# Kernel tuning notes

Hardware: AMD Instinct MI355X
Metric: run time of the kernel (lower is better)

Reference implementation:

```python
import jax, jax.numpy as jnp
import numpy as np

B, C_IN, H, W = 2, 128, 96, 320
CQ = C_IN // 4   # q/k channels = 32
D = 32           # number of disparities


def _groupnorm1(x, w, b, eps=1e-5):
    # GroupNorm with 1 group == LayerNorm over (C,H,W) per sample, per-channel affine
    mu = x.mean(axis=(1, 2, 3), keepdims=True)
    var = x.var(axis=(1, 2, 3), keepdims=True)
    return (x - mu) / jnp.sqrt(var + eps) * w[None, :, None, None] + b[None, :, None, None]


def _warp_volume(x, disp, directs):
    # Faithful to affine_grid + grid_sample(bilinear, border, align_corners=True)
    # with a pure horizontal shift: pixel offset = disp * direct * (W-1).
    Bx, C, Hx, Wx = x.shape
    d = directs.reshape(Bx, 1, 1)                       # [B,1,1]
    j = jnp.arange(Wx, dtype=x.dtype)
    pos = j[None, None, :] + disp[None, :, None] * d * (Wx - 1)   # [B,D,W]
    pos = jnp.clip(pos, 0.0, Wx - 1)                    # border padding
    x0 = jnp.clip(jnp.floor(pos).astype(jnp.int32), 0, Wx - 1)
    x1 = jnp.minimum(x0 + 1, Wx - 1)
    t = pos - x0.astype(x.dtype)                        # [B,D,W]

    def per_b(xb, i0, i1, tb):
        g0 = xb[:, :, i0]                                # [C,H,D,W]
        g1 = xb[:, :, i1]
        return g0 * (1.0 - tb) + g1 * tb

    warped = jax.vmap(per_b)(x, x0, x1, t)               # [B,C,H,D,W]
    return jnp.moveaxis(warped, 3, 4)                    # [B,C,H,W,D]


def setup_inputs() -> dict:
    key = jax.random.key(0)
    ks = jax.random.split(key, 12)
    s = lambda i, shape: jax.random.normal(ks[i], shape, jnp.float32) * 0.05
    return {
        "t_feat": jax.random.normal(ks[0], (B, C_IN, H, W), jnp.float32),
        "s_feat": jax.random.normal(ks[1], (B, C_IN, H, W), jnp.float32),
        "directs": jnp.ones((B, 1, 1, 1), jnp.float32),
        "disp": jnp.arange(D, dtype=jnp.float32) * 0.01,   # norm_disp_range
        "q_w": s(2, (CQ, C_IN)), "q_b": jnp.zeros((CQ,), jnp.float32),
        "k_w": s(3, (CQ, C_IN)), "k_b": jnp.zeros((CQ,), jnp.float32),
        "cf_w": s(4, (1, 1, 3, 3, 3)), "cf_b": jnp.zeros((1,), jnp.float32),
        "nt_w": jnp.ones((C_IN,), jnp.float32), "nt_b": jnp.zeros((C_IN,), jnp.float32),
        "nc_w": jnp.ones((D,), jnp.float32), "nc_b": jnp.zeros((D,), jnp.float32),
        "ce_w": s(5, (C_IN, D)), "ce_b": jnp.zeros((C_IN,), jnp.float32),
        "fa_w": s(6, (1, 2 * C_IN)), "fa_b": jnp.zeros((1,), jnp.float32),
        "rc_w": s(7, (C_IN, C_IN, 3, 3)), "rc_b": jnp.zeros((C_IN,), jnp.float32),
        "se_w1": s(8, (C_IN // 16, C_IN)),
        "se_w2": s(9, (C_IN, C_IN // 16)),
    }


def reference(t_feat, s_feat, directs, disp, q_w, q_b, k_w, k_b, cf_w, cf_b,
              nt_w, nt_b, nc_w, nc_b, ce_w, ce_b, fa_w, fa_b, rc_w, rc_b,
              se_w1, se_w2):
    eps = 1e-12
    # 1x1 q/k projections
    q = jnp.einsum('oc,bchw->bohw', q_w, t_feat) + q_b[None, :, None, None]
    k = jnp.einsum('oc,bchw->bohw', k_w, s_feat) + k_b[None, :, None, None]

    # per-disparity warp -> [B,Cq,H,W,D]
    warped = _warp_volume(k, disp, directs)

    # DAV with patch_size=1: per-pixel cosine similarity over channels
    qn = q / jnp.maximum(jnp.linalg.norm(q, axis=1, keepdims=True), eps)
    kn = warped / jnp.maximum(jnp.linalg.norm(warped, axis=1, keepdims=True), eps)
    sim = jnp.einsum('bchw,bchwd->bdhw', qn, kn)          # [B,D,H,W]

    # 3x3x3 cost filter (Conv3d 1->1, padding 1)
    cost = jax.lax.conv_general_dilated(
        sim[:, None], cf_w, (1, 1, 1), [(1, 1)] * 3,
        dimension_numbers=('NCDHW', 'OIDHW', 'NCDHW'))[:, 0] + cf_b[0]
    norm_cost = jax.nn.softmax(cost, axis=1)              # softmax over D

    t_n = _groupnorm1(t_feat, nt_w, nt_b)
    c_n = _groupnorm1(norm_cost, nc_w, nc_b)
    cost_feat = jnp.einsum('od,bdhw->bohw', ce_w, c_n) + ce_b[None, :, None, None]

    fusion_in = jnp.concatenate([t_n, cost_feat], axis=1)
    alpha = jax.nn.sigmoid(jnp.einsum('oc,bchw->bohw', fa_w, fusion_in)
                           + fa_b[None, :, None, None])
    fused = alpha * t_n + (1.0 - alpha) * cost_feat       # same spatial size, no interp

    # redu: reflection-pad 3x3 conv -> SE -> ELU
    xp = jnp.pad(fused, ((0, 0), (0, 0), (1, 1), (1, 1)), mode='reflect')
    x = jax.lax.conv_general_dilated(
        xp, rc_w, (1, 1), 'VALID',
        dimension_numbers=('NCHW', 'OIHW', 'NCHW')) + rc_b[None, :, None, None]
    y = x.mean(axis=(2, 3))                               # [B,C]
    y = jax.nn.relu(y @ se_w1.T)
    y = jax.nn.sigmoid(y @ se_w2.T)
    x = jax.nn.elu(x * y[:, :, None, None])
    return (x, norm_cost)
```

## Files before the change

### kernel.cpp

```cpp
#include <hip/hip_runtime.h>
#include <stdint.h>

#define CC    128
#define CQn   32
#define DD    32
#define IMG_H 96
#define IMG_W 320
#define HW    30720
#define NPIX  61440

#define OFF_Q     0
#define OFF_K     3932160
#define OFF_SIM   7864320
#define OFF_NCP   15728640
#define OFF_FUSED 0
#define OFF_WC    19660800
#define OFF_WQK   19955712
#define OFF_AP    19972096
#define OFF_MISC  19988480
#define OFF_ST    20000768

typedef _Float16 half_t;
typedef _Float16 f16x2 __attribute__((ext_vector_type(2)));
typedef _Float16 f16x8 __attribute__((ext_vector_type(8)));
typedef float    f32x4 __attribute__((ext_vector_type(4)));

__device__ __forceinline__ float fdot2f(f16x2 a, f16x2 b, float c){
#if __has_builtin(__builtin_amdgcn_fdot2)
  return __builtin_amdgcn_fdot2(a, b, c, false);
#else
  return c + (float)a.x*(float)b.x + (float)a.y*(float)b.y;
#endif
}

__global__ __launch_bounds__(256) void k0_prep(
    const float* __restrict__ rc_w, const float* __restrict__ q_w, const float* __restrict__ k_w,
    const float* __restrict__ ce_w, const float* __restrict__ ce_b,
    const float* __restrict__ fa_w, const float* __restrict__ nt_w, const float* __restrict__ nt_b,
    half_t* __restrict__ wconv, half_t* __restrict__ wqk, float* __restrict__ gbuf){
  int blk = blockIdx.x, tid = threadIdx.x;
  if (blk < 576){
    int idx = blk * 256 + tid;
    int j = idx & 7;
    int o = (idx >> 3) & 127;
    int g = idx >> 10;
    int kq = g & 3, q4 = (g >> 2) & 3, pos = g >> 4;
    int c = q4*32 + kq*8 + j;
    wconv[idx] = (half_t)rc_w[(o*128 + c)*9 + pos];
  } else if (blk < 608){
    int idx = (blk - 576) * 256 + tid;
    wqk[idx] = (half_t)(idx < 4096 ? q_w[idx] : k_w[idx - 4096]);
  } else {
    int t = tid;
    if (t < 32){
      float a = 0.f;
      for (int o = 0; o < 128; o++) a += fa_w[128 + o] * ce_w[o * 32 + t];
      gbuf[t] = a;
    } else if (t == 32){
      float a = 0.f;
      for (int o = 0; o < 128; o++) a += fa_w[128 + o] * ce_b[o];
      gbuf[32] = a;
    } else if (t == 33){
      float a = 0.f;
      for (int c = 0; c < 128; c++) a += fa_w[c] * nt_w[c];
      gbuf[33] = a;
    } else if (t == 34){
      float a = 0.f;
      for (int c = 0; c < 128; c++) a += fa_w[c] * nt_b[c];
      gbuf[34] = a;
    }
  }
}

__global__ __launch_bounds__(256) void k1_qk(
    const float* __restrict__ t_feat, const float* __restrict__ s_feat,
    const half_t* __restrict__ wqk, const float* __restrict__ q_b, const float* __restrict__ k_b,
    half_t* __restrict__ qbuf, half_t* __restrict__ kbuf,
    double* __restrict__ tsum, double* __restrict__ tsq){
  __shared__ half_t feat[128 * 136];
  __shared__ float red1[4], red2[4];
  __shared__ float qbl[32], kbl[32];
  int tid = threadIdx.x;
  int b = blockIdx.x / 240;
  int pix0 = (blockIdx.x % 240) * 128;
  int lane = tid & 63, wid = tid >> 6;
  int quad = lane >> 4, l15 = lane & 15;
  if (tid < 32){ qbl[tid] = q_b[tid]; kbl[tid] = k_b[tid]; }
  int px_s = tid & 127, hf = tid >> 7;

  for (int phase = 0; phase < 2; phase++){
    const float* src = (phase == 0 ? t_feat : s_feat) + (size_t)b * CC * HW + pix0 + px_s;
    float s1 = 0.f, s2 = 0.f;
    for (int c = hf * 64; c < hf * 64 + 64; c += 2){
      float v0 = src[c * HW], v1 = src[(c + 1) * HW];
      if (phase == 0){ s1 += v0 + v1; s2 += v0 * v0 + v1 * v1; }
      *(f16x2*)&feat[px_s * 136 + c] = f16x2{(half_t)v0, (half_t)v1};
    }
    if (phase == 0){
      #pragma unroll
      for (int off = 32; off > 0; off >>= 1){ s1 += __shfl_down(s1, off, 64); s2 += __shfl_down(s2, off, 64); }
      if (lane == 0){ red1[wid] = s1; red2[wid] = s2; }
    }
    __syncthreads();
    if (phase == 0 && tid == 0){
      atomicAdd(&tsum[b], (double)red1[0] + red1[1] + red1[2] + red1[3]);
      atomicAdd(&tsq[b],  (double)red2[0] + red2[1] + red2[2] + red2[3]);
    }
    const half_t* W = wqk + phase * 4096;
    f32x4 acc[2][2];
    #pragma unroll
    for (int m = 0; m < 2; m++){ acc[m][0] = (f32x4){0,0,0,0}; acc[m][1] = (f32x4){0,0,0,0}; }
    #pragma unroll
    for (int q4 = 0; q4 < 4; q4++){
      f16x8 a0 = *(const f16x8*)&W[(l15) * 128 + q4*32 + quad*8];
      f16x8 a1 = *(const f16x8*)&W[(16 + l15) * 128 + q4*32 + quad*8];
      #pragma unroll
      for (int nt = 0; nt < 2; nt++){
        f16x8 bf = *(const f16x8*)&feat[(wid*32 + nt*16 + l15) * 136 + q4*32 + quad*8];
        acc[0][nt] = __builtin_amdgcn_mfma_f32_16x16x32_f16(a0, bf, acc[0][nt], 0, 0, 0);
        acc[1][nt] = __builtin_amdgcn_mfma_f32_16x16x32_f16(a1, bf, acc[1][nt], 0, 0, 0);
      }
    }
    const float* bl = phase == 0 ? qbl : kbl;
    #pragma unroll
    for (int m = 0; m < 2; m++)
      #pragma unroll
      for (int nt = 0; nt < 2; nt++)
        #pragma unroll
        for (int r = 0; r < 4; r++){
          int o = m*16 + quad*4 + r;
          feat[(wid*32 + nt*16 + l15) * 136 + o] = (half_t)(acc[m][nt][r] + bl[o]);
        }
    __syncthreads();
    {
      half_t* dst = (phase == 0 ? qbuf : kbuf) + (size_t)(b * HW + pix0 + px_s) * 32;
      if (hf == 0){
        uint4* d4 = (uint4*)dst;
        const uint4* s4 = (const uint4*)&feat[px_s * 136];
        d4[0] = s4[0]; d4[1] = s4[1]; d4[2] = s4[2]; d4[3] = s4[3];
      }
    }
    __syncthreads();
  }
}

__global__ __launch_bounds__(320) void k2_sim(
    const half_t* __restrict__ qbuf, const half_t* __restrict__ kbuf,
    const float* __restrict__ directs, const float* __restrict__ disp,
    float* __restrict__ sim){
  __shared__ uint4 klds4[320 * 5];
  __shared__ float displ[32];
  int tid = threadIdx.x;
  int b = blockIdx.y, h = blockIdx.x;
  for (int u = tid; u < 1280; u += 320){
    int x = u >> 2, j = u & 3;
    klds4[x * 5 + j] = ((const uint4*)(kbuf + (size_t)(b * HW + h * IMG_W + x) * 32))[j];
  }
  if (tid < 32) displ[tid] = disp[tid];
  __syncthreads();
  int w = tid;
  float direct = directs[b];
  union U16 { uint4 u4[4]; f16x2 h2[16]; };
  U16 qu;
  {
    const uint4* qp = (const uint4*)(qbuf + (size_t)(b * HW + h * IMG_W + w) * 32);
    qu.u4[0] = qp[0]; qu.u4[1] = qp[1]; qu.u4[2] = qp[2]; qu.u4[3] = qp[3];
  }
  float nq2 = 0.f;
  #pragma unroll
  for (int i = 0; i < 16; i++) nq2 = fdot2f(qu.h2[i], qu.h2[i], nq2);
  float inv_q = 1.0f / fmaxf(sqrtf(nq2), 1e-12f);
  float* simb = sim + (size_t)b * DD * HW + h * IMG_W + w;
  for (int d = 0; d < 32; d++){
    float pos = (float)w + displ[d] * direct * (float)(IMG_W - 1);
    pos = fminf(fmaxf(pos, 0.0f), (float)(IMG_W - 1));
    int x0 = (int)pos;
    int x1 = min(x0 + 1, IMG_W - 1);
    half_t tt = (half_t)(pos - (float)x0);
    f16x2 t2 = {tt, tt};
    U16 k0u, k1u;
    const uint4* r0 = &klds4[x0 * 5];
    const uint4* r1 = &klds4[x1 * 5];
    #pragma unroll
    for (int j = 0; j < 4; j++){ k0u.u4[j] = r0[j]; k1u.u4[j] = r1[j]; }
    float dot = 0.f, n2 = 0.f;
    #pragma unroll
    for (int i = 0; i < 16; i++){
      f16x2 wv = k0u.h2[i] + t2 * (k1u.h2[i] - k0u.h2[i]);
      dot = fdot2f(wv, qu.h2[i], dot);
      n2  = fdot2f(wv, wv, n2);
    }
    simb[d * HW] = dot * inv_q / fmaxf(sqrtf(n2), 1e-12f);
  }
}

__global__ __launch_bounds__(320) void k3_cost(
    const float* __restrict__ sim, const float* __restrict__ cf_w,
    float* __restrict__ norm_cost, half_t* __restrict__ ncp,
    double* __restrict__ csum, double* __restrict__ csq){
  __shared__ float w3[27];
  __shared__ float red1[5], red2[5];
  int tid = threadIdx.x;
  if (tid < 27) w3[tid] = cf_w[tid];
  __syncthreads();
  int b = blockIdx.y, h = blockIdx.x, w = tid;
  float cost[32];
  #pragma unroll
  for (int d = 0; d < 32; d++) cost[d] = 0.f;
  const float* sb = sim + (size_t)b * DD * HW;
  #pragma unroll
  for (int i = 0; i < 3; i++){
    int hh = h + i - 1;
    if (hh < 0 || hh >= IMG_H) continue;
    #pragma unroll
    for (int j = 0; j < 3; j++){
      int ww = w + j - 1;
      bool ok = (ww >= 0 && ww < IMG_W);
      const float* col = sb + hh * IMG_W + (ok ? ww : 0);
      float w0 = w3[0*9 + i*3 + j], w1 = w3[1*9 + i*3 + j], w2 = w3[2*9 + i*3 + j];
      #pragma unroll
      for (int e = 0; e < 32; e++){
        float v = ok ? col[e * HW] : 0.f;
        if (e < 31) cost[e+1] += w0 * v;
        cost[e] += w1 * v;
        if (e > 0)  cost[e-1] += w2 * v;
      }
    }
  }
  float mx = cost[0];
  #pragma unroll
  for (int d = 1; d < 32; d++) mx = fmaxf(mx, cost[d]);
  float s = 0.f;
  #pragma unroll
  for (int d = 0; d < 32; d++){ cost[d] = expf(cost[d] - mx); s += cost[d]; }
  float inv = 1.0f / s;
  float s1 = 0.f, s2 = 0.f;
  float* nb = norm_cost + (size_t)b * DD * HW + h * IMG_W + w;
  #pragma unroll
  for (int d = 0; d < 32; d++){
    float nc = cost[d] * inv;
    cost[d] = nc;
    nb[d * HW] = nc;
    s1 += nc; s2 += nc * nc;
  }
  {
    union { f16x2 h2[16]; uint4 u4[4]; } u;
    #pragma unroll
    for (int i = 0; i < 16; i++) u.h2[i] = f16x2{(half_t)cost[2*i], (half_t)cost[2*i+1]};
    uint4* dst = (uint4*)(ncp + (size_t)(b * HW + h * IMG_W + w) * 32);
    dst[0] = u.u4[0]; dst[1] = u.u4[1]; dst[2] = u.u4[2]; dst[3] = u.u4[3];
  }
  #pragma unroll
  for (int off = 32; off > 0; off >>= 1){ s1 += __shfl_down(s1, off, 64); s2 += __shfl_down(s2, off, 64); }
  int lane = tid & 63, wid = tid >> 6;
  if (lane == 0){ red1[wid] = s1; red2[wid] = s2; }
  __syncthreads();
  if (tid == 0){
    double a1 = 0, a2 = 0;
    for (int i = 0; i < 5; i++){ a1 += red1[i]; a2 += red2[i]; }
    atomicAdd(&csum[b], a1);
    atomicAdd(&csq[b], a2);
  }
}

__global__ __launch_bounds__(256) void k35_prep(
    const float* __restrict__ ce_w, const float* __restrict__ ce_b,
    const float* __restrict__ nt_w, const float* __restrict__ nt_b,
    const float* __restrict__ nc_w, const float* __restrict__ nc_b,
    const float* __restrict__ fa_w, const float* __restrict__ fa_b,
    const double* __restrict__ tsum, const double* __restrict__ tsq,
    const double* __restrict__ csum, const double* __restrict__ csq,
    const float* __restrict__ gbuf, half_t* __restrict__ ap, float* __restrict__ biasp,
    float* __restrict__ tnA, float* __restrict__ tnB, float* __restrict__ h1g,
    float* __restrict__ gp, float* __restrict__ zc){
  int t = threadIdx.x;
  int b = t >> 7, o = t & 127;
  float mu_t  = (float)(tsum[b] * (1.0 / (128.0 * HW)));
  float var_t = (float)(tsq[b]  * (1.0 / (128.0 * HW))) - mu_t * mu_t;
  float inv_t = 1.0f / sqrtf(var_t + 1e-5f);
  float mu_c  = (float)(csum[b] * (1.0 / (32.0 * HW)));
  float var_c = (float)(csq[b]  * (1.0 / (32.0 * HW))) - mu_c * mu_c;
  float inv_c = 1.0f / sqrtf(var_c + 1e-5f);
  float bias = ce_b[o];
  half_t* apo = ap + (size_t)(b * 128 + o) * 32;
  for (int d = 0; d < 32; d++){
    float wv = ce_w[o * 32 + d];
    bias += wv * (nc_b[d] - nc_w[d] * inv_c * mu_c);
    apo[d] = (half_t)(wv * nc_w[d] * inv_c);
  }
  biasp[b * 128 + o] = bias;
  tnA[b * 128 + o] = inv_t * nt_w[o];
  tnB[b * 128 + o] = nt_b[o] - mu_t * inv_t * nt_w[o];
  h1g[b * 128 + o] = fa_w[o] * nt_w[o] * inv_t;
  if (o < 32) gp[b * 32 + o] = gbuf[o] * nc_w[o] * inv_c;
  if (o == 0){
    float z = gbuf[32] + gbuf[34] - mu_t * inv_t * gbuf[33] + fa_b[0];
    for (int d = 0; d < 32; d++) z += gbuf[d] * (nc_b[d] - nc_w[d] * inv_c * mu_c);
    zc[b] = z;
  }
}

__global__ __launch_bounds__(256) void k4_fuse(
    const float* __restrict__ t_feat, const half_t* __restrict__ ncp,
    const half_t* __restrict__ ap, const float* __restrict__ biasp,
    const float* __restrict__ tnA, const float* __restrict__ tnB,
    const float* __restrict__ h1g, const float* __restrict__ gp,
    const float* __restrict__ zc, half_t* __restrict__ fused){
  __shared__ half_t cf[128 * 136];
  __shared__ float alphas[128];
  __shared__ float zred[256];
  __shared__ float biasl[128], tnAl[128], tnBl[128];
  int tid = threadIdx.x;
  int b = blockIdx.x / 240;
  int pix0 = (blockIdx.x % 240) * 128;
  int lane = tid & 63, wid = tid >> 6, quad = lane >> 4, l15 = lane & 15;
  if (tid < 128){
    biasl[tid] = biasp[b * 128 + tid];
    tnAl[tid] = tnA[b * 128 + tid];
    tnBl[tid] = tnB[b * 128 + tid];
  }
  {
    int px = tid & 127, hf = tid >> 7;
    const float* tf = t_feat + (size_t)b * CC * HW + pix0 + px;
    float z = 0.f;
    for (int c = hf * 64; c < hf * 64 + 64; c++) z += h1g[b * 128 + c] * tf[c * HW];
    if (hf == 0){
      const half_t* np = ncp + (size_t)(b * HW + pix0 + px) * 32;
      for (int d = 0; d < 32; d++) z += gp[b * 32 + d] * (float)np[d];
    }
    zred[tid] = z;
  }
  __syncthreads();
  if (tid < 128){
    float z = zred[tid] + zred[tid + 128] + zc[b];
    alphas[tid] = 1.0f / (1.0f + expf(-z));
  }
  f32x4 acc[8][2];
  #pragma unroll
  for (int mt = 0; mt < 8; mt++){ acc[mt][0] = (f32x4){0,0,0,0}; acc[mt][1] = (f32x4){0,0,0,0}; }
  f16x8 bfr[2];
  #pragma unroll
  for (int nt = 0; nt < 2; nt++)
    bfr[nt] = *(const f16x8*)&ncp[(size_t)(b * HW + pix0 + wid*32 + nt*16 + l15) * 32 + quad * 8];
  #pragma unroll
  for (int mt = 0; mt < 8; mt++){
    f16x8 a = *(const f16x8*)&ap[(size_t)(b * 128 + mt*16 + l15) * 32 + quad * 8];
    acc[mt][0] = __builtin_amdgcn_mfma_f32_16x16x32_f16(a, bfr[0], acc[mt][0], 0, 0, 0);
    acc[mt][1] = __builtin_amdgcn_mfma_f32_16x16x32_f16(a, bfr[1], acc[mt][1], 0, 0, 0);
  }
  #pragma unroll
  for (int mt = 0; mt < 8; mt++)
    #pragma unroll
    for (int nt = 0; nt < 2; nt++)
      #pragma unroll
      for (int r = 0; r < 4; r++){
        int o = mt*16 + quad*4 + r;
        cf[(wid*32 + nt*16 + l15) * 136 + o] = (half_t)(acc[mt][nt][r] + biasl[o]);
      }
  __syncthreads();
  {
    int px = (wid & 1) * 64 + lane;
    int ob = (wid >> 1) * 64;
    float al = alphas[px];
    const float* tf = t_feat + (size_t)b * CC * HW + pix0 + px;
    for (int oo = 0; oo < 64; oo++){
      int o = ob + oo;
      float tn = tf[o * HW] * tnAl[o] + tnBl[o];
      float c = (float)cf[px * 136 + o];
      cf[px * 136 + o] = (half_t)(al * (tn - c) + c);
    }
  }
  __syncthreads();
  {
    int px = tid >> 1, hf = tid & 1;
    const uint4* srow = (const uint4*)&cf[px * 136 + hf * 64];
    uint4* drow = (uint4*)(fused + (size_t)(b * HW + pix0 + px) * 128 + hf * 64);
    #pragma unroll
    for (int j = 0; j < 8; j++) drow[j] = srow[j];
  }
}

__global__ __launch_bounds__(256, 2) void k5_conv(
    const half_t* __restrict__ fused, const half_t* __restrict__ wconv,
    const float* __restrict__ rc_b, float* __restrict__ xout, float* __restrict__ ysum){
  __shared__ half_t patch[6 * 34 * 136];
  __shared__ float rcb[128];
  int tid = threadIdx.x;
  int b = blockIdx.z;
  int h0 = blockIdx.y * 4;
  int w0 = blockIdx.x * 32;
  int lane = tid & 63, wid = tid >> 6, quad = lane >> 4, l15 = lane & 15;
  if (tid < 128) rcb[tid] = rc_b[tid];

  for (int idx = tid; idx < 204 * 16; idx += 256){
    int pp = idx >> 4, j = idx & 15;
    int r = pp / 34, col = pp - r * 34;
    int hs = h0 + r - 1;  hs = hs < 0 ? 1 : (hs >= IMG_H ? 2*IMG_H - 2 - hs : hs);
    int ws = w0 + col - 1; ws = ws < 0 ? 1 : (ws >= IMG_W ? 2*IMG_W - 2 - ws : ws);
    const uint4* s = (const uint4*)(fused + (size_t)(b * HW + hs * IMG_W + ws) * 128) + j;
    *((uint4*)&patch[(r * 34 + col) * 136] + j) = *s;
  }
  __syncthreads();

  f32x4 acc[2][8];
  #pragma unroll
  for (int mt = 0; mt < 2; mt++)
    #pragma unroll
    for (int nt = 0; nt < 8; nt++) acc[mt][nt] = (f32x4){0.f,0.f,0.f,0.f};

  for (int pos = 0; pos < 9; pos++){
    int kh = pos / 3;
    int kw2 = pos - kh * 3;
    #pragma unroll
    for (int q4 = 0; q4 < 4; q4++){
      const half_t* wrow = wconv + ((size_t)(pos*16 + q4*4 + quad) * 128 + wid*32 + l15) * 8;
      f16x8 A0 = *(const f16x8*)wrow;
      f16x8 A1 = *(const f16x8*)(wrow + 128);
      #pragma unroll
      for (int nt = 0; nt < 8; nt++){
        int hrow = nt >> 1, whalf = nt & 1;
        f16x8 B = *(const f16x8*)&patch[((hrow + kh)*34 + whalf*16 + l15 + kw2)*136 + q4*32 + quad*8];
        acc[0][nt] = __builtin_amdgcn_mfma_f32_16x16x32_f16(A0, B, acc[0][nt], 0, 0, 0);
        acc[1][nt] = __builtin_amdgcn_mfma_f32_16x16x32_f16(A1, B, acc[1][nt], 0, 0, 0);
      }
    }
  }

  #pragma unroll
  for (int mt = 0; mt < 2; mt++){
    float ysl[4] = {0.f, 0.f, 0.f, 0.f};
    #pragma unroll
    for (int nt = 0; nt < 8; nt++){
      int hh = h0 + (nt >> 1);
      int ww = w0 + (nt & 1)*16 + l15;
      #pragma unroll
      for (int r = 0; r < 4; r++){
        int o = wid*32 + mt*16 + quad*4 + r;
        float v = acc[mt][nt][r] + rcb[o];
        xout[((size_t)(b * CC + o) * IMG_H + hh) * IMG_W + ww] = v;
        float rv = v;
        rv += __shfl_xor(rv, 1, 64);
        rv += __shfl_xor(rv, 2, 64);
        rv += __shfl_xor(rv, 4, 64);
        rv += __shfl_xor(rv, 8, 64);
        ysl[r] += rv;
      }
    }
    if (l15 == 0){
      #pragma unroll
      for (int r = 0; r < 4; r++) atomicAdd(&ysum[b * CC + wid*32 + mt*16 + quad*4 + r], ysl[r]);
    }
  }
}

__global__ __launch_bounds__(256) void k6_se(
    const float* __restrict__ ysum, const float* __restrict__ se_w1,
    const float* __restrict__ se_w2, float* __restrict__ sescale){
  __shared__ float ym[256];
  __shared__ float y1[16];
  int t = threadIdx.x;
  ym[t] = ysum[t] * (1.0f / (float)HW);
  __syncthreads();
  if (t < 16){
    int b = t >> 3, j = t & 7;
    float a = 0.f;
    for (int o = 0; o < 128; o++) a += ym[b * 128 + o] * se_w1[j * 128 + o];
    y1[t] = fmaxf(a, 0.f);
  }
  __syncthreads();
  int b = t >> 7, o = t & 127;
  float a = 0.f;
  #pragma unroll
  for (int j = 0; j < 8; j++) a += y1[b * 8 + j] * se_w2[o * 8 + j];
  sescale[t] = 1.0f / (1.0f + expf(-a));
}

__global__ __launch_bounds__(256) void k7_elu(float* __restrict__ x, const float* __restrict__ sescale){
  int i4 = blockIdx.x * 256 + threadIdx.x;
  float4* xp = (float4*)x;
  float4 v = xp[i4];
  float s = sescale[i4 / 7680];
  float a = v.x * s, bb = v.y * s, c = v.z * s, d = v.w * s;
  v.x = a  > 0.f ? a  : expm1f(a);
  v.y = bb > 0.f ? bb : expm1f(bb);
  v.z = c  > 0.f ? c  : expm1f(c);
  v.w = d  > 0.f ? d  : expm1f(d);
  xp[i4] = v;
}

extern "C" void kernel_launch(void* const* d_in, const int* in_sizes, int n_in,
                              void* d_out, int out_size, void* d_ws, size_t ws_size,
                              hipStream_t stream){
  const float* t_feat = (const float*)d_in[0];
  const float* s_feat = (const float*)d_in[1];
  const float* directs = (const float*)d_in[2];
  const float* disp   = (const float*)d_in[3];
  const float* q_w = (const float*)d_in[4];
  const float* q_b = (const float*)d_in[5];
  const float* k_w = (const float*)d_in[6];
  const float* k_b = (const float*)d_in[7];
  const float* cf_w = (const float*)d_in[8];
  const float* nt_w = (const float*)d_in[10];
  const float* nt_b = (const float*)d_in[11];
  const float* nc_w = (const float*)d_in[12];
  const float* nc_b = (const float*)d_in[13];
  const float* ce_w = (const float*)d_in[14];
  const float* ce_b = (const float*)d_in[15];
  const float* fa_w = (const float*)d_in[16];
  const float* fa_b = (const float*)d_in[17];
  const float* rc_w = (const float*)d_in[18];
  const float* rc_b = (const float*)d_in[19];
  const float* se_w1 = (const float*)d_in[20];
  const float* se_w2 = (const float*)d_in[21];

  char* ws = (char*)d_ws;
  half_t* qbuf  = (half_t*)(ws + OFF_Q);
  half_t* kbuf  = (half_t*)(ws + OFF_K);
  float*  sim   = (float*)(ws + OFF_SIM);
  half_t* ncp   = (half_t*)(ws + OFF_NCP);
  half_t* fused = (half_t*)(ws + OFF_FUSED);
  half_t* wconv = (half_t*)(ws + OFF_WC);
  half_t* wqk   = (half_t*)(ws + OFF_WQK);
  half_t* ap    = (half_t*)(ws + OFF_AP);
  float*  biasp = (float*)(ws + OFF_MISC);
  float*  tnA   = (float*)(ws + OFF_MISC + 1024);
  float*  tnB   = (float*)(ws + OFF_MISC + 2048);
  float*  h1g   = (float*)(ws + OFF_MISC + 3072);
  float*  gp    = (float*)(ws + OFF_MISC + 4096);
  float*  zc    = (float*)(ws + OFF_MISC + 4352);
  char* st = ws + OFF_ST;
  double* tsum = (double*)(st + 0);
  double* tsq  = (double*)(st + 16);
  double* csum = (double*)(st + 32);
  double* csq  = (double*)(st + 48);
  float* ysum  = (float*)(st + 64);
  float* sescale = (float*)(st + 1088);
  float* gbuf  = (float*)(st + 2112);

  float* xout = (float*)d_out;
  float* norm_cost = (float*)d_out + 7864320;

  hipMemsetAsync(st, 0, 1088, stream);
  k0_prep<<<610, 256, 0, stream>>>(rc_w, q_w, k_w, ce_w, ce_b, fa_w, nt_w, nt_b, wconv, wqk, gbuf);
  k1_qk<<<480, 256, 0, stream>>>(t_feat, s_feat, wqk, q_b, k_b, qbuf, kbuf, tsum, tsq);
  k2_sim<<<dim3(96, 2), 320, 0, stream>>>(qbuf, kbuf, directs, disp, sim);
  k3_cost<<<dim3(96, 2), 320, 0, stream>>>(sim, cf_w, norm_cost, ncp, csum, csq);
  k35_prep<<<1, 256, 0, stream>>>(ce_w, ce_b, nt_w, nt_b, nc_w, nc_b, fa_w, fa_b,
                                  tsum, tsq, csum, csq, gbuf, ap, biasp, tnA, tnB, h1g, gp, zc);
  k4_fuse<<<480, 256, 0, stream>>>(t_feat, ncp, ap, biasp, tnA, tnB, h1g, gp, zc, fused);
  k5_conv<<<dim3(10, 24, 2), 256, 0, stream>>>(fused, wconv, rc_b, xout, ysum);
  k6_se<<<1, 256, 0, stream>>>(ysum, se_w1, se_w2, sescale);
  k7_elu<<<7680, 256, 0, stream>>>(xout, sescale);
}
```

Before: 305.5 us.

## Split disparity loop across threads, fuse t_feat normalize, retile conv with weight prefetch

k2_sim doubles the block to 640 threads, with each half handling 16 of the 32 disparities, to get more parallelism out of only 192 blocks. k4_fuse reads t_feat once, writes the normalized values into a new shared buffer, and blends alpha directly in the MFMA epilogue, removing the second global read of t_feat and one pass over shared memory. k5_conv changes the patch layout to channel-chunk-major to cut LDS bank conflicts. It also retiles each warp to 64 outputs by 16 pixels so each B fragment feeds 4 MFMAs, and prefetches the next weight fragments in registers. The costs are extra LDS in k4, which may lower occupancy, and more accumulator and weight registers in k5.

```diff
diff --git a/kernel.cpp b/kernel.cpp
--- a/kernel.cpp
+++ b/kernel.cpp
@@ -144,7 +144,7 @@
   }
 }
 
-__global__ __launch_bounds__(320) void k2_sim(
+__global__ __launch_bounds__(640) void k2_sim(
     const half_t* __restrict__ qbuf, const half_t* __restrict__ kbuf,
     const float* __restrict__ directs, const float* __restrict__ disp,
     float* __restrict__ sim){
@@ -152,13 +152,15 @@
   __shared__ float displ[32];
   int tid = threadIdx.x;
   int b = blockIdx.y, h = blockIdx.x;
-  for (int u = tid; u < 1280; u += 320){
+  for (int u = tid; u < 1280; u += 640){
     int x = u >> 2, j = u & 3;
     klds4[x * 5 + j] = ((const uint4*)(kbuf + (size_t)(b * HW + h * IMG_W + x) * 32))[j];
   }
   if (tid < 32) displ[tid] = disp[tid];
   __syncthreads();
-  int w = tid;
+  int dh = tid >= 320 ? 1 : 0;
+  int w = tid - dh * 320;
+  int d0 = dh * 16;
   float direct = directs[b];
   union U16 { uint4 u4[4]; f16x2 h2[16]; };
   U16 qu;
@@ -171,7 +173,7 @@
   for (int i = 0; i < 16; i++) nq2 = fdot2f(qu.h2[i], qu.h2[i], nq2);
   float inv_q = 1.0f / fmaxf(sqrtf(nq2), 1e-12f);
   float* simb = sim + (size_t)b * DD * HW + h * IMG_W + w;
-  for (int d = 0; d < 32; d++){
+  for (int d = d0; d < d0 + 16; d++){
     float pos = (float)w + displ[d] * direct * (float)(IMG_W - 1);
     pos = fminf(fmaxf(pos, 0.0f), (float)(IMG_W - 1));
     int x0 = (int)pos;
@@ -307,6 +309,7 @@
     const float* __restrict__ h1g, const float* __restrict__ gp,
     const float* __restrict__ zc, half_t* __restrict__ fused){
   __shared__ half_t cf[128 * 136];
+  __shared__ half_t tnb[128 * 136];
   __shared__ float alphas[128];
   __shared__ float zred[256];
   __shared__ float biasl[128], tnAl[128], tnBl[128];
@@ -319,11 +322,17 @@
     tnAl[tid] = tnA[b * 128 + tid];
     tnBl[tid] = tnB[b * 128 + tid];
   }
+  __syncthreads();
   {
     int px = tid & 127, hf = tid >> 7;
     const float* tf = t_feat + (size_t)b * CC * HW + pix0 + px;
+    const float* hg = h1g + b * 128;
     float z = 0.f;
-    for (int c = hf * 64; c < hf * 64 + 64; c++) z += h1g[b * 128 + c] * tf[c * HW];
+    for (int c = hf * 64; c < hf * 64 + 64; c++){
+      float tv = tf[c * HW];
+      z += hg[c] * tv;
+      tnb[px * 136 + c] = (half_t)(tv * tnAl[c] + tnBl[c]);
+    }
     if (hf == 0){
       const half_t* np = ncp + (size_t)(b * HW + pix0 + px) * 32;
       for (int d = 0; d < 32; d++) z += gp[b * 32 + d] * (float)np[d];
@@ -348,27 +357,20 @@
     acc[mt][0] = __builtin_amdgcn_mfma_f32_16x16x32_f16(a, bfr[0], acc[mt][0], 0, 0, 0);
     acc[mt][1] = __builtin_amdgcn_mfma_f32_16x16x32_f16(a, bfr[1], acc[mt][1], 0, 0, 0);
   }
-  #pragma unroll
-  for (int mt = 0; mt < 8; mt++)
-    #pragma unroll
-    for (int nt = 0; nt < 2; nt++)
+  __syncthreads();
+  #pragma unroll
+  for (int nt = 0; nt < 2; nt++){
+    int px = wid*32 + nt*16 + l15;
+    float al = alphas[px];
+    #pragma unroll
+    for (int mt = 0; mt < 8; mt++)
       #pragma unroll
       for (int r = 0; r < 4; r++){
         int o = mt*16 + quad*4 + r;
-        cf[(wid*32 + nt*16 + l15) * 136 + o] = (half_t)(acc[mt][nt][r] + biasl[o]);
+        float cfv = acc[mt][nt][r] + biasl[o];
+        float tn = (float)tnb[px * 136 + o];
+        cf[px * 136 + o] = (half_t)(al * (tn - cfv) + cfv);
       }
-  __syncthreads();
-  {
-    int px = (wid & 1) * 64 + lane;
-    int ob = (wid >> 1) * 64;
-    float al = alphas[px];
-    const float* tf = t_feat + (size_t)b * CC * HW + pix0 + px;
-    for (int oo = 0; oo < 64; oo++){
-      int o = ob + oo;
-      float tn = tf[o * HW] * tnAl[o] + tnBl[o];
-      float c = (float)cf[px * 136 + o];
-      cf[px * 136 + o] = (half_t)(al * (tn - c) + c);
-    }
   }
   __syncthreads();
   {
@@ -383,59 +385,72 @@
 __global__ __launch_bounds__(256, 2) void k5_conv(
     const half_t* __restrict__ fused, const half_t* __restrict__ wconv,
     const float* __restrict__ rc_b, float* __restrict__ xout, float* __restrict__ ysum){
-  __shared__ half_t patch[6 * 34 * 136];
+  __shared__ __align__(16) half_t patch[16][6][34][8];
   __shared__ float rcb[128];
   int tid = threadIdx.x;
   int b = blockIdx.z;
   int h0 = blockIdx.y * 4;
   int w0 = blockIdx.x * 32;
   int lane = tid & 63, wid = tid >> 6, quad = lane >> 4, l15 = lane & 15;
+  int oh = wid >> 1, ph = wid & 1;
   if (tid < 128) rcb[tid] = rc_b[tid];
 
-  for (int idx = tid; idx < 204 * 16; idx += 256){
-    int pp = idx >> 4, j = idx & 15;
-    int r = pp / 34, col = pp - r * 34;
-    int hs = h0 + r - 1;  hs = hs < 0 ? 1 : (hs >= IMG_H ? 2*IMG_H - 2 - hs : hs);
-    int ws = w0 + col - 1; ws = ws < 0 ? 1 : (ws >= IMG_W ? 2*IMG_W - 2 - ws : ws);
-    const uint4* s = (const uint4*)(fused + (size_t)(b * HW + hs * IMG_W + ws) * 128) + j;
-    *((uint4*)&patch[(r * 34 + col) * 136] + j) = *s;
-  }
-  __syncthreads();
-
-  f32x4 acc[2][8];
-  #pragma unroll
-  for (int mt = 0; mt < 2; mt++)
-    #pragma unroll
-    for (int nt = 0; nt < 8; nt++) acc[mt][nt] = (f32x4){0.f,0.f,0.f,0.f};
-
-  for (int pos = 0; pos < 9; pos++){
-    int kh = pos / 3;
-    int kw2 = pos - kh * 3;
-    #pragma unroll
-    for (int q4 = 0; q4 < 4; q4++){
-      const half_t* wrow = wconv + ((size_t)(pos*16 + q4*4 + quad) * 128 + wid*32 + l15) * 8;
-      f16x8 A0 = *(const f16x8*)wrow;
-      f16x8 A1 = *(const f16x8*)(wrow + 128);
-      #pragma unroll
-      for (int nt = 0; nt < 8; nt++){
-        int hrow = nt >> 1, whalf = nt & 1;
-        f16x8 B = *(const f16x8*)&patch[((hrow + kh)*34 + whalf*16 + l15 + kw2)*136 + q4*32 + quad*8];
-        acc[0][nt] = __builtin_amdgcn_mfma_f32_16x16x32_f16(A0, B, acc[0][nt], 0, 0, 0);
-        acc[1][nt] = __builtin_amdgcn_mfma_f32_16x16x32_f16(A1, B, acc[1][nt], 0, 0, 0);
+  {
+    int j = tid >> 4, pl = tid & 15;
+    #pragma unroll
+    for (int it = 0; it < 13; it++){
+      int pp = it * 16 + pl;
+      if (pp < 204){
+        int r = pp / 34, col = pp - r * 34;
+        int hs = h0 + r - 1;  hs = hs < 0 ? 1 : (hs >= IMG_H ? 2*IMG_H - 2 - hs : hs);
+        int ws = w0 + col - 1; ws = ws < 0 ? 1 : (ws >= IMG_W ? 2*IMG_W - 2 - ws : ws);
+        *(uint4*)&patch[j][r][col][0] =
+            *((const uint4*)(fused + (size_t)(b * HW + hs * IMG_W + ws) * 128) + j);
       }
     }
   }
-
-  #pragma unroll
-  for (int mt = 0; mt < 2; mt++){
+  __syncthreads();
+
+  f32x4 acc[4][4];
+  #pragma unroll
+  for (int mt = 0; mt < 4; mt++)
+    #pragma unroll
+    for (int nt = 0; nt < 4; nt++) acc[mt][nt] = (f32x4){0.f,0.f,0.f,0.f};
+
+  const half_t* wbase = wconv + ((size_t)quad * 128 + oh * 64 + l15) * 8;
+  f16x8 Acur[4], Anext[4];
+  #pragma unroll
+  for (int mt = 0; mt < 4; mt++) Anext[mt] = *(const f16x8*)(wbase + mt * 128);
+  for (int s = 0; s < 36; s++){
+    #pragma unroll
+    for (int mt = 0; mt < 4; mt++) Acur[mt] = Anext[mt];
+    if (s < 35){
+      const half_t* wp = wbase + (size_t)(s + 1) * 4096;
+      #pragma unroll
+      for (int mt = 0; mt < 4; mt++) Anext[mt] = *(const f16x8*)(wp + mt * 128);
+    }
+    int pos = s >> 2, q4 = s & 3;
+    int kh = (pos * 11) >> 5;
+    int kw = pos - kh * 3;
+    #pragma unroll
+    for (int nt = 0; nt < 4; nt++){
+      f16x8 B = *(const f16x8*)&patch[q4*4 + quad][nt + kh][ph*16 + l15 + kw][0];
+      #pragma unroll
+      for (int mt = 0; mt < 4; mt++)
+        acc[mt][nt] = __builtin_amdgcn_mfma_f32_16x16x32_f16(Acur[mt], B, acc[mt][nt], 0, 0, 0);
+    }
+  }
+
+  #pragma unroll
+  for (int mt = 0; mt < 4; mt++){
     float ysl[4] = {0.f, 0.f, 0.f, 0.f};
     #pragma unroll
-    for (int nt = 0; nt < 8; nt++){
-      int hh = h0 + (nt >> 1);
-      int ww = w0 + (nt & 1)*16 + l15;
+    for (int nt = 0; nt < 4; nt++){
+      int hh = h0 + nt;
+      int ww = w0 + ph*16 + l15;
       #pragma unroll
       for (int r = 0; r < 4; r++){
-        int o = wid*32 + mt*16 + quad*4 + r;
+        int o = oh*64 + mt*16 + quad*4 + r;
         float v = acc[mt][nt][r] + rcb[o];
         xout[((size_t)(b * CC + o) * IMG_H + hh) * IMG_W + ww] = v;
         float rv = v;
@@ -448,7 +463,8 @@
     }
     if (l15 == 0){
       #pragma unroll
-      for (int r = 0; r < 4; r++) atomicAdd(&ysum[b * CC + wid*32 + mt*16 + quad*4 + r], ysl[r]);
+      for (int r = 0; r < 4; r++)
+        atomicAdd(&ysum[b * CC + oh*64 + mt*16 + quad*4 + r], ysl[r]);
     }
   }
 }
@@ -543,7 +559,7 @@
   hipMemsetAsync(st, 0, 1088, stream);
   k0_prep<<<610, 256, 0, stream>>>(rc_w, q_w, k_w, ce_w, ce_b, fa_w, nt_w, nt_b, wconv, wqk, gbuf);
   k1_qk<<<480, 256, 0, stream>>>(t_feat, s_feat, wqk, q_b, k_b, qbuf, kbuf, tsum, tsq);
-  k2_sim<<<dim3(96, 2), 320, 0, stream>>>(qbuf, kbuf, directs, disp, sim);
+  k2_sim<<<dim3(96, 2), 640, 0, stream>>>(qbuf, kbuf, directs, disp, sim);
   k3_cost<<<dim3(96, 2), 320, 0, stream>>>(sim, cf_w, norm_cost, ncp, csum, csq);
   k35_prep<<<1, 256, 0, stream>>>(ce_w, ce_b, nt_w, nt_b, nc_w, nc_b, fa_w, fa_b,
                                   tsum, tsq, csum, csq, gbuf, ap, biasp, tnA, tnB, h1g, gp, zc);
```

Result: slower. 324.9 us (+6.4%).
